# Kernel tuning notes

Measured on AMD Instinct MI355X. Metric: run time of the kernel, lower is better.

Reference implementation:

```python
import jax, jax.numpy as jnp
import numpy as np

MEM = 50   # memory_size
LA = 5     # look_ahead
EPS = 1e-5


def _tap_conv(h, taps, pad_left, pad_right):
    """Channel-independent temporal correlation with scalar taps.
    h: [B, L, H]; taps: [K]. out[t] = sum_j taps[j] * h[t + j - pad_left] (zero-padded).
    Returns [B, L + pad_left + pad_right - K + 1, H]."""
    B, L, H = h.shape
    K = taps.shape[0]
    xc = h.transpose(0, 2, 1).reshape(B * H, 1, L)
    k = taps.reshape(1, 1, K)
    out = jax.lax.conv_general_dilated(xc, k, (1,), [(pad_left, pad_right)],
                                       dimension_numbers=("NCH", "OIH", "NCH"))
    Lo = out.shape[-1]
    return out.reshape(B, H, Lo).transpose(0, 2, 1)


def _forward(x, W_lin, b_lin, mem_w, la_w, gamma, beta):
    B, L, D = x.shape
    H = W_lin.shape[0]
    # h = Linear(x); dropout is identity in eval mode
    h = jnp.einsum("bld,hd->blh", x, W_lin) + b_lin  # [B, L, H]

    # Source math: matmul(states^T, W[:k]).sum(-1) == sum_m states[:,m,:] * W[m,:].sum()
    wm = mem_w.sum(axis=-1)  # [MEM] scalar tap weights
    wf = la_w.sum(axis=-1)   # [LA]

    # --- memory (past) context ---
    # For t >= MEM: mem[t] = sum_j wm[j] * h[t - MEM + j]  (lag alignment)
    mem_conv = _tap_conv(h, wm, MEM, 0)[:, :L]  # [B, L, H]
    # For t < MEM: taps align to absolute times 0..t-1 with weights wm[0..t-1]
    wh = h[:, :MEM] * wm[None, :, None]                 # [B, MEM, H]
    pre = jnp.cumsum(wh, axis=1)                        # pre[t] = sum_{j<=t} wm[j] h[j]
    pref = jnp.concatenate([jnp.zeros((B, 1, H), h.dtype), pre[:, :MEM - 1]], axis=1)
    mem = jnp.concatenate([pref, mem_conv[:, MEM:]], axis=1)  # [B, L, H]

    # --- look-ahead (future) context ---
    # fut[t] = sum_j wf[j] * h[t + 1 + j], zero beyond L (truncation == zero pad)
    fut = _tap_conv(h, wf, 0, LA)[:, 1:L + 1]  # [B, L, H]

    out = h + mem + fut
    # LayerNorm over last dim
    mu = out.mean(axis=-1, keepdims=True)
    var = out.var(axis=-1, keepdims=True)
    out = (out - mu) * jax.lax.rsqrt(var + EPS) * gamma + beta
    return out


def setup_inputs() -> dict:
    key = jax.random.key(0)
    ks = jax.random.split(key, 5)
    B, L, D, H = 8, 2048, 1024, 2048
    x = jax.random.normal(ks[0], (B, L, D), jnp.float32)
    W_lin = jax.random.normal(ks[1], (H, D), jnp.float32) * (1.0 / np.sqrt(D))
    b_lin = jax.random.normal(ks[2], (H,), jnp.float32) * 0.01
    mem_w = jax.random.normal(ks[3], (MEM, H), jnp.float32)
    la_w = jax.random.normal(ks[4], (LA, H), jnp.float32)
    gamma = jnp.ones((H,), jnp.float32)
    beta = jnp.zeros((H,), jnp.float32)
    return {"x": x, "W_lin": W_lin, "b_lin": b_lin, "mem_w": mem_w,
            "la_w": la_w, "gamma": gamma, "beta": beta}


def reference(x, W_lin, b_lin, mem_w, la_w, gamma, beta):
    return _forward(x, W_lin, b_lin, mem_w, la_w, gamma, beta)
```

## Files before the change

### kernel.cpp

```cpp
#include <hip/hip_runtime.h>

typedef unsigned short u16;
typedef unsigned int u32;
typedef short bf16x8 __attribute__((ext_vector_type(8)));
typedef float f32x4 __attribute__((ext_vector_type(4)));

#define Mdim 16384
#define Ndim 2048
#define Kdim 1024
#define Lseq 2048
#define Bb   8

__device__ __forceinline__ void gload_lds16(const void* g, void* l) {
    __builtin_amdgcn_global_load_lds(
        (const __attribute__((address_space(1))) u32*)(g),
        (__attribute__((address_space(3))) u32*)(l), 16, 0, 0);
}

__device__ __forceinline__ u16 f32_to_bf16(float f) {
    u32 u = __builtin_bit_cast(u32, f);
    u += 0x7FFFu + ((u >> 16) & 1u);
    return (u16)(u >> 16);
}

__global__ __launch_bounds__(256) void cast_f32_bf16(
        const float* __restrict__ in, u16* __restrict__ out, int n8) {
    int i = blockIdx.x * 256 + threadIdx.x;
    if (i >= n8) return;
    const float4* p = (const float4*)(in + (size_t)i * 8);
    float4 a = p[0], b = p[1];
    float v[8] = {a.x, a.y, a.z, a.w, b.x, b.y, b.z, b.w};
    u32 o[4];
#pragma unroll
    for (int j = 0; j < 4; ++j) {
        u32 lo = f32_to_bf16(v[2 * j]);
        u32 hi = f32_to_bf16(v[2 * j + 1]);
        o[j] = lo | (hi << 16);
    }
    uint4 ov = make_uint4(o[0], o[1], o[2], o[3]);
    *(uint4*)(out + (size_t)i * 8) = ov;
}

__global__ __launch_bounds__(256) void taps_kernel(
        const float* __restrict__ mem_w, const float* __restrict__ la_w,
        float* __restrict__ cw) {
    int k = blockIdx.x;
    if (k == 50) {
        if (threadIdx.x == 0) cw[50] = 1.0f;
        return;
    }
    const float* src = (k < 50) ? (mem_w + (size_t)k * Ndim)
                                : (la_w + (size_t)(k - 51) * Ndim);
    float s = 0.f;
    for (int i = threadIdx.x; i < Ndim; i += 256) s += src[i];
#pragma unroll
    for (int off = 32; off; off >>= 1) s += __shfl_down(s, off);
    __shared__ float part[4];
    if ((threadIdx.x & 63) == 0) part[threadIdx.x >> 6] = s;
    __syncthreads();
    if (threadIdx.x == 0) cw[k] = part[0] + part[1] + part[2] + part[3];
}

__global__ __launch_bounds__(256) void gemm_bias(
        const u16* __restrict__ A, const u16* __restrict__ Bw,
        const float* __restrict__ bias, u16* __restrict__ C) {
    __shared__ __align__(16) u16 sA[2][128 * 32];
    __shared__ __align__(16) u16 sB[2][128 * 32];
    const int tid = threadIdx.x;
    const int bn = blockIdx.x, bm = blockIdx.y;
    const int w = tid >> 6, lane = tid & 63;
    const int wr = w >> 1, wc = w & 1;
    const int ln = lane & 15, kq = lane >> 4;

    f32x4 acc[4][4] = {};

    auto stage = [&](int buf, int k0) {
#pragma unroll
        for (int p = 0; p < 2; ++p) {
            int c = p * 256 + tid;
            int row = c >> 2, cg = c & 3;
            gload_lds16(A + (size_t)(bm * 128 + row) * Kdim + k0 + cg * 8,
                        &sA[buf][c * 8]);
            gload_lds16(Bw + (size_t)(bn * 128 + row) * Kdim + k0 + cg * 8,
                        &sB[buf][c * 8]);
        }
    };

    stage(0, 0);
    int cur = 0;
    const int NK = Kdim / 32;
    for (int kt = 0; kt < NK; ++kt) {
        __syncthreads();
        if (kt + 1 < NK) stage(cur ^ 1, (kt + 1) * 32);
        bf16x8 af[4], bf[4];
#pragma unroll
        for (int i = 0; i < 4; ++i) {
            af[i] = *(const bf16x8*)&sA[cur][(wr * 64 + i * 16 + ln) * 32 + kq * 8];
            bf[i] = *(const bf16x8*)&sB[cur][(wc * 64 + i * 16 + ln) * 32 + kq * 8];
        }
#pragma unroll
        for (int i = 0; i < 4; ++i)
#pragma unroll
            for (int j = 0; j < 4; ++j)
                acc[i][j] = __builtin_amdgcn_mfma_f32_16x16x32_bf16(
                    af[i], bf[j], acc[i][j], 0, 0, 0);
        cur ^= 1;
    }

    const int colb = bn * 128 + wc * 64;
    const int rowb = bm * 128 + wr * 64;
#pragma unroll
    for (int j = 0; j < 4; ++j) {
        int col = colb + j * 16 + ln;
        float bv = bias[col];
#pragma unroll
        for (int i = 0; i < 4; ++i) {
            int row0 = rowb + i * 16 + kq * 4;
#pragma unroll
            for (int r = 0; r < 4; ++r) {
                float v = acc[i][j][r] + bv;
                C[(size_t)(row0 + r) * Ndim + col] = f32_to_bf16(v);
            }
        }
    }
}

__global__ __launch_bounds__(256) void conv_ln(
        const u16* __restrict__ h, const float* __restrict__ cwg,
        const float* __restrict__ gamma, const float* __restrict__ beta,
        float* __restrict__ out) {
    const int tid = threadIdx.x;
    const int tb = blockIdx.x * 8;
    const int b = blockIdx.y;

    __shared__ float scw[70];
    __shared__ float red[4][8][2];
    if (tid < 70) scw[tid] = (tid >= 7 && tid < 63) ? cwg[tid - 7] : 0.f;
    __syncthreads();

    const u16* hb = h + (size_t)b * Lseq * Ndim;
    const int ch = tid * 8;
    float acc[8][8] = {};

    if (tb >= 50) {
        const int lrend = min(62, (Lseq - 1) - (tb - 50));
        const u16* rp = hb + (size_t)(tb - 50) * Ndim + ch;
        for (int lr = 0; lr <= lrend; ++lr) {
            uint4 u = *(const uint4*)rp;
            rp += Ndim;
            float hv[8];
            hv[0] = __builtin_bit_cast(float, u.x << 16);
            hv[1] = __builtin_bit_cast(float, u.x & 0xFFFF0000u);
            hv[2] = __builtin_bit_cast(float, u.y << 16);
            hv[3] = __builtin_bit_cast(float, u.y & 0xFFFF0000u);
            hv[4] = __builtin_bit_cast(float, u.z << 16);
            hv[5] = __builtin_bit_cast(float, u.z & 0xFFFF0000u);
            hv[6] = __builtin_bit_cast(float, u.w << 16);
            hv[7] = __builtin_bit_cast(float, u.w & 0xFFFF0000u);
#pragma unroll
            for (int t2 = 0; t2 < 8; ++t2) {
                float wgt = scw[lr - t2 + 7];
#pragma unroll
                for (int j = 0; j < 8; ++j)
                    acc[t2][j] = fmaf(wgt, hv[j], acc[t2][j]);
            }
        }
    } else {
        const int rmax = tb + 12;
        const u16* rp = hb + ch;
        for (int r = 0; r <= rmax; ++r) {
            uint4 u = *(const uint4*)rp;
            rp += Ndim;
            float hv[8];
            hv[0] = __builtin_bit_cast(float, u.x << 16);
            hv[1] = __builtin_bit_cast(float, u.x & 0xFFFF0000u);
            hv[2] = __builtin_bit_cast(float, u.y << 16);
            hv[3] = __builtin_bit_cast(float, u.y & 0xFFFF0000u);
            hv[4] = __builtin_bit_cast(float, u.z << 16);
            hv[5] = __builtin_bit_cast(float, u.z & 0xFFFF0000u);
            hv[6] = __builtin_bit_cast(float, u.w << 16);
            hv[7] = __builtin_bit_cast(float, u.w & 0xFFFF0000u);
#pragma unroll
            for (int t2 = 0; t2 < 8; ++t2) {
                int t = tb + t2;
                float wgt;
                if (t >= 50) {
                    int wi = r - t + 50;
                    wgt = ((unsigned)wi <= 55u) ? scw[wi + 7] : 0.f;
                } else if (r < t) {
                    wgt = scw[r + 7];
                } else {
                    int d = r - t;
                    wgt = (d <= 5) ? scw[50 + d + 7] : 0.f;
                }
#pragma unroll
                for (int j = 0; j < 8; ++j)
                    acc[t2][j] = fmaf(wgt, hv[j], acc[t2][j]);
            }
        }
    }

    float g[8], be[8];
    *(float4*)&g[0] = *(const float4*)(gamma + ch);
    *(float4*)&g[4] = *(const float4*)(gamma + ch + 4);
    *(float4*)&be[0] = *(const float4*)(beta + ch);
    *(float4*)&be[4] = *(const float4*)(beta + ch + 4);

    float s1v[8], s2v[8];
#pragma unroll
    for (int t2 = 0; t2 < 8; ++t2) {
        float s1 = 0.f, s2 = 0.f;
#pragma unroll
        for (int j = 0; j < 8; ++j) {
            s1 += acc[t2][j];
            s2 += acc[t2][j] * acc[t2][j];
        }
        s1v[t2] = s1;
        s2v[t2] = s2;
    }
#pragma unroll
    for (int off = 32; off; off >>= 1) {
#pragma unroll
        for (int t2 = 0; t2 < 8; ++t2) {
            s1v[t2] += __shfl_down(s1v[t2], off);
            s2v[t2] += __shfl_down(s2v[t2], off);
        }
    }
    const int wv = tid >> 6, lane = tid & 63;
    if (lane == 0) {
#pragma unroll
        for (int t2 = 0; t2 < 8; ++t2) {
            red[wv][t2][0] = s1v[t2];
            red[wv][t2][1] = s2v[t2];
        }
    }
    __syncthreads();
    const float inv = 1.0f / (float)Ndim;
#pragma unroll
    for (int t2 = 0; t2 < 8; ++t2) {
        float S1 = red[0][t2][0] + red[1][t2][0] + red[2][t2][0] + red[3][t2][0];
        float S2 = red[0][t2][1] + red[1][t2][1] + red[2][t2][1] + red[3][t2][1];
        float mu = S1 * inv;
        float var = S2 * inv - mu * mu;
        float rs = rsqrtf(var + 1e-5f);
        size_t base = ((size_t)(b * Lseq + tb + t2)) * Ndim + ch;
        float4 o0, o1;
        o0.x = (acc[t2][0] - mu) * rs * g[0] + be[0];
        o0.y = (acc[t2][1] - mu) * rs * g[1] + be[1];
        o0.z = (acc[t2][2] - mu) * rs * g[2] + be[2];
        o0.w = (acc[t2][3] - mu) * rs * g[3] + be[3];
        o1.x = (acc[t2][4] - mu) * rs * g[4] + be[4];
        o1.y = (acc[t2][5] - mu) * rs * g[5] + be[5];
        o1.z = (acc[t2][6] - mu) * rs * g[6] + be[6];
        o1.w = (acc[t2][7] - mu) * rs * g[7] + be[7];
        *(float4*)(out + base) = o0;
        *(float4*)(out + base + 4) = o1;
    }
}

extern "C" void kernel_launch(void* const* d_in, const int* in_sizes, int n_in,
                              void* d_out, int out_size, void* d_ws, size_t ws_size,
                              hipStream_t stream) {
    const float* x     = (const float*)d_in[0];
    const float* W     = (const float*)d_in[1];
    const float* b_lin = (const float*)d_in[2];
    const float* mem_w = (const float*)d_in[3];
    const float* la_w  = (const float*)d_in[4];
    const float* gamma = (const float*)d_in[5];
    const float* beta  = (const float*)d_in[6];
    float* out = (float*)d_out;

    u16* xb = (u16*)d_ws;
    u16* wb = xb + (size_t)16777216;
    u16* hb = wb + (size_t)2097152;
    float* cw = (float*)(hb + (size_t)33554432);

    taps_kernel<<<dim3(56), dim3(256), 0, stream>>>(mem_w, la_w, cw);
    cast_f32_bf16<<<dim3(8192), dim3(256), 0, stream>>>(x, xb, 2097152);
    cast_f32_bf16<<<dim3(1024), dim3(256), 0, stream>>>(W, wb, 262144);
    gemm_bias<<<dim3(16, 128), dim3(256), 0, stream>>>(xb, wb, b_lin, hb);
    conv_ln<<<dim3(256, 8), dim3(256), 0, stream>>>(hb, cw, gamma, beta, out);
}
```

Before: 378.3 us.

## Rewrite GEMM with 256x256 tiles, 8 waves, swizzled LDS and staged prefetch

Replaces the 128x128, 4-wave bf16 GEMM with a 256x256 tile per 512-thread block using a 64-wide K step and 128KB of double-buffered LDS. Global-to-LDS loads for the next tiles are split into quarter stages that are interleaved with MFMA work. An XOR swizzle is used to avoid LDS bank conflicts, and a block-id remap improves L2 locality. This aims to raise arithmetic intensity and overlap memory with compute, at the cost of one block per CU and more complex barrier and waitcnt ordering.

```diff
diff --git a/kernel.cpp b/kernel.cpp
--- a/kernel.cpp
+++ b/kernel.cpp
@@ -5,11 +5,10 @@
 typedef short bf16x8 __attribute__((ext_vector_type(8)));
 typedef float f32x4 __attribute__((ext_vector_type(4)));
 
-#define Mdim 16384
 #define Ndim 2048
 #define Kdim 1024
 #define Lseq 2048
-#define Bb   8
+#define NT   16
 
 __device__ __forceinline__ void gload_lds16(const void* g, void* l) {
     __builtin_amdgcn_global_load_lds(
@@ -22,6 +21,8 @@
     u += 0x7FFFu + ((u >> 16) & 1u);
     return (u16)(u >> 16);
 }
+
+__device__ __forceinline__ u32 swz(u32 x) { return x ^ (((x >> 9) & 1u) << 5); }
 
 __global__ __launch_bounds__(256) void cast_f32_bf16(
         const float* __restrict__ in, u16* __restrict__ out, int n8) {
@@ -61,68 +62,111 @@
     if (threadIdx.x == 0) cw[k] = part[0] + part[1] + part[2] + part[3];
 }
 
-__global__ __launch_bounds__(256) void gemm_bias(
+__global__ __launch_bounds__(512, 1) void gemm8(
         const u16* __restrict__ A, const u16* __restrict__ Bw,
         const float* __restrict__ bias, u16* __restrict__ C) {
-    __shared__ __align__(16) u16 sA[2][128 * 32];
-    __shared__ __align__(16) u16 sB[2][128 * 32];
+    __shared__ __align__(16) u16 smem[65536];
+    char* sb = (char*)smem;
+
     const int tid = threadIdx.x;
-    const int bn = blockIdx.x, bm = blockIdx.y;
     const int w = tid >> 6, lane = tid & 63;
-    const int wr = w >> 1, wc = w & 1;
     const int ln = lane & 15, kq = lane >> 4;
-
-    f32x4 acc[4][4] = {};
-
-    auto stage = [&](int buf, int k0) {
+    const int wr = w >> 2, wc = w & 3;
+
+    const int id0 = blockIdx.x;
+    const int id = (id0 & 7) * 64 + (id0 >> 3);
+    const int bm = id >> 3, bn = id & 7;
+
+    const u32 aoff = (u32)(wr * 64 + ln) * 128 + (u32)kq * 16;
+    const u32 boff = (u32)(wc * 32 + ln) * 128 + (u32)kq * 16;
+
+    f32x4 acc[8][4] = {};
+
+    auto stage = [&](int kt2, int which) {
+        const int ah = which & 1;
+        const bool isB = (which >> 1) != 0;
+        const u16* src = isB ? Bw : A;
+        const int rowbase = (isB ? bn * 256 : bm * 256) + ah * 128;
+        const u32 dbase = (u32)(kt2 & 1) * 65536u + (isB ? 32768u : 0u) + (u32)ah * 16384u;
 #pragma unroll
         for (int p = 0; p < 2; ++p) {
-            int c = p * 256 + tid;
-            int row = c >> 2, cg = c & 3;
-            gload_lds16(A + (size_t)(bm * 128 + row) * Kdim + k0 + cg * 8,
-                        &sA[buf][c * 8]);
-            gload_lds16(Bw + (size_t)(bn * 128 + row) * Kdim + k0 + cg * 8,
-                        &sB[buf][c * 8]);
+            u32 off = (u32)(p * 512 + tid) * 16;
+            u32 soff = swz(off);
+            u32 srow = soff >> 7, scol = (soff & 127u) >> 1;
+            gload_lds16(src + (size_t)(rowbase + (int)srow) * Kdim + kt2 * 64 + (int)scol,
+                        sb + dbase + off);
         }
     };
 
-    stage(0, 0);
-    int cur = 0;
-    const int NK = Kdim / 32;
-    for (int kt = 0; kt < NK; ++kt) {
-        __syncthreads();
-        if (kt + 1 < NK) stage(cur ^ 1, (kt + 1) * 32);
-        bf16x8 af[4], bf[4];
-#pragma unroll
-        for (int i = 0; i < 4; ++i) {
-            af[i] = *(const bf16x8*)&sA[cur][(wr * 64 + i * 16 + ln) * 32 + kq * 8];
-            bf[i] = *(const bf16x8*)&sB[cur][(wc * 64 + i * 16 + ln) * 32 + kq * 8];
-        }
-#pragma unroll
-        for (int i = 0; i < 4; ++i)
-#pragma unroll
-            for (int j = 0; j < 4; ++j)
-                acc[i][j] = __builtin_amdgcn_mfma_f32_16x16x32_bf16(
-                    af[i], bf[j], acc[i][j], 0, 0, 0);
-        cur ^= 1;
-    }
-
-    const int colb = bn * 128 + wc * 64;
-    const int rowb = bm * 128 + wr * 64;
-#pragma unroll
-    for (int j = 0; j < 4; ++j) {
-        int col = colb + j * 16 + ln;
-        float bv = bias[col];
-#pragma unroll
-        for (int i = 0; i < 4; ++i) {
-            int row0 = rowb + i * 16 + kq * 4;
-#pragma unroll
-            for (int r = 0; r < 4; ++r) {
-                float v = acc[i][j][r] + bv;
-                C[(size_t)(row0 + r) * Ndim + col] = f32_to_bf16(v);
+    stage(0, 0); stage(0, 1); stage(0, 2); stage(0, 3);
+    stage(1, 0); stage(1, 2);
+    asm volatile("s_waitcnt vmcnt(4)");
+    __builtin_amdgcn_sched_barrier(0);
+    __builtin_amdgcn_s_barrier();
+
+    for (int kt = 0; kt < NT; ++kt) {
+        const u32 bufb = (u32)(kt & 1) * 65536u;
+#pragma unroll
+        for (int q = 0; q < 4; ++q) {
+            const int mh = q >> 1, nh = q & 1;
+            bf16x8 a[4][2], b[2][2];
+#pragma unroll
+            for (int m = 0; m < 4; ++m)
+#pragma unroll
+                for (int ks = 0; ks < 2; ++ks)
+                    a[m][ks] = *(const bf16x8*)(sb + bufb + (u32)mh * 16384u +
+                                                swz(aoff + (u32)m * 2048u + (u32)ks * 64u));
+#pragma unroll
+            for (int n = 0; n < 2; ++n)
+#pragma unroll
+                for (int ks = 0; ks < 2; ++ks)
+                    b[n][ks] = *(const bf16x8*)(sb + bufb + 32768u + (u32)nh * 16384u +
+                                                swz(boff + (u32)n * 2048u + (u32)ks * 64u));
+            if (q == 0)      { if (kt + 1 < NT) stage(kt + 1, 1); }
+            else if (q == 1) { if (kt + 1 < NT) stage(kt + 1, 3); }
+            else if (q == 2) { if (kt + 2 < NT) stage(kt + 2, 0); }
+            else             { if (kt + 2 < NT) stage(kt + 2, 2); }
+            __builtin_amdgcn_s_barrier();
+            asm volatile("s_waitcnt lgkmcnt(0)");
+            __builtin_amdgcn_sched_barrier(0);
+            __builtin_amdgcn_s_setprio(1);
+#pragma unroll
+            for (int m = 0; m < 4; ++m)
+#pragma unroll
+                for (int n = 0; n < 2; ++n) {
+                    acc[mh * 4 + m][nh * 2 + n] = __builtin_amdgcn_mfma_f32_16x16x32_bf16(
+                        a[m][0], b[n][0], acc[mh * 4 + m][nh * 2 + n], 0, 0, 0);
+                    acc[mh * 4 + m][nh * 2 + n] = __builtin_amdgcn_mfma_f32_16x16x32_bf16(
+                        a[m][1], b[n][1], acc[mh * 4 + m][nh * 2 + n], 0, 0, 0);
+                }
+            __builtin_amdgcn_s_setprio(0);
+            if (q == 3) {
+                asm volatile("s_waitcnt vmcnt(4)");
+                __builtin_amdgcn_sched_barrier(0);
             }
-        }
-    }
+            __builtin_amdgcn_s_barrier();
+        }
+    }
+
+    const int colbase = bn * 256 + wc * 32;
+    const int rowbase = bm * 256 + wr * 64;
+#pragma unroll
+    for (int nh = 0; nh < 2; ++nh)
+#pragma unroll
+        for (int n = 0; n < 2; ++n) {
+            int col = colbase + nh * 128 + n * 16 + ln;
+            float bv = bias[col];
+#pragma unroll
+            for (int mh = 0; mh < 2; ++mh)
+#pragma unroll
+                for (int m = 0; m < 4; ++m) {
+                    int row0 = rowbase + mh * 128 + m * 16 + kq * 4;
+                    f32x4 v = acc[mh * 4 + m][nh * 2 + n];
+#pragma unroll
+                    for (int r = 0; r < 4; ++r)
+                        C[(size_t)(row0 + r) * Ndim + col] = f32_to_bf16(v[r] + bv);
+                }
+        }
 }
 
 __global__ __launch_bounds__(256) void conv_ln(
@@ -278,6 +322,6 @@
     taps_kernel<<<dim3(56), dim3(256), 0, stream>>>(mem_w, la_w, cw);
     cast_f32_bf16<<<dim3(8192), dim3(256), 0, stream>>>(x, xb, 2097152);
     cast_f32_bf16<<<dim3(1024), dim3(256), 0, stream>>>(W, wb, 262144);
-    gemm_bias<<<dim3(16, 128), dim3(256), 0, stream>>>(xb, wb, b_lin, hb);
+    gemm8<<<dim3(512), dim3(512), 0, stream>>>(xb, wb, b_lin, hb);
     conv_ln<<<dim3(256, 8), dim3(256), 0, stream>>>(hb, cw, gamma, beta, out);
 }
```

Result: no change. 376.8 us (-0.4%).
